# Kernel tuning notes

Hardware: AMD Instinct MI355X
Metric: run time of the kernel (lower is better)

The kernel has to match this reference:

```python
import jax, jax.numpy as jnp
import numpy as np

NX, NH, NY, T = 128, 512, 1, 16384


def setup_inputs() -> dict:
    key = jax.random.key(0)
    ks = jax.random.split(key, 10)
    s = 0.01
    return {
        "x_t": jax.random.normal(ks[0], (T, 1), dtype=jnp.float32),
        "Wf": jax.random.normal(ks[1], (NH, NX), dtype=jnp.float32) * s,
        "Uf": jax.random.normal(ks[2], (NH, NH), dtype=jnp.float32) * s,
        "bf": jnp.zeros((NH,), dtype=jnp.float32),
        "Wi": jax.random.normal(ks[3], (NH, NX), dtype=jnp.float32) * s,
        "Ui": jax.random.normal(ks[4], (NH, NH), dtype=jnp.float32) * s,
        "bi": jnp.zeros((NH,), dtype=jnp.float32),
        "Wo": jax.random.normal(ks[5], (NH, NX), dtype=jnp.float32) * s,
        "Uo": jax.random.normal(ks[6], (NH, NH), dtype=jnp.float32) * s,
        "bo": jnp.zeros((NH,), dtype=jnp.float32),
        "Wc": jax.random.normal(ks[7], (NH, NX), dtype=jnp.float32) * s,
        "Uc": jax.random.normal(ks[8], (NH, NH), dtype=jnp.float32) * s,
        "bc": jnp.zeros((NH,), dtype=jnp.float32),
        "Ahy": jax.random.normal(ks[9], (NY, NH), dtype=jnp.float32) * s,
        "by": jnp.zeros((NY,), dtype=jnp.float32),
    }


def reference(x_t, Wf, Uf, bf, Wi, Ui, bi, Wo, Uo, bo, Wc, Uc, bc, Ahy, by):
    # x_t: (T, 1) univariate series; sliding windows of length Nx feed each step.
    Tlen = x_t.shape[0]
    Nx = Wf.shape[1]
    Nh = Wf.shape[0]
    steps = Tlen - Nx  # number of recurrent steps

    x = x_t[:, 0]  # (T,)
    idx = jnp.arange(steps)[:, None] + jnp.arange(Nx)[None, :]
    Xw = x[idx]  # (steps, Nx) sliding windows

    # Precompute input projections for all steps (batched GEMMs).
    xf = Xw @ Wf.T + bf  # (steps, Nh)
    xi = Xw @ Wi.T + bi
    xo = Xw @ Wo.T + bo
    xc = Xw @ Wc.T + bc

    def step(carry, inp):
        h, c = carry
        xf_t, xi_t, xo_t, xc_t = inp
        f = jax.nn.sigmoid(xf_t + Uf @ h)
        i = jax.nn.sigmoid(xi_t + Ui @ h)
        o = jax.nn.sigmoid(xo_t + Uo @ h)
        g = jnp.tanh(xc_t + Uc @ h)
        c = f * c + i * g
        h = o * jnp.tanh(c)
        mu = Ahy @ h + by  # (Ny,)
        return (h, c), mu

    init = (jnp.zeros((Nh,), x_t.dtype), jnp.zeros((Nh,), x_t.dtype))
    _, mu = jax.lax.scan(step, init, (xf, xi, xo, xc))
    return mu  # (steps, Ny) == (T-Nx, 1), matching torch's stack(...).unsqueeze(1)
```

## Files before the change

kernel.cpp:

```cpp
#include <hip/hip_runtime.h>

#define NHID 512
#define NXW  128
#define TLEN 16384
#define STEPS (TLEN - NXW)
#define G    32
#define B    512
#define RPW  16
#define RSLOTS 8

#define FOR4(M)  M(0) M(1) M(2) M(3)
#define FOR16(M) M(0) M(1) M(2) M(3) M(4) M(5) M(6) M(7) \
                 M(8) M(9) M(10) M(11) M(12) M(13) M(14) M(15)

__device__ __forceinline__ float sigmoid_f(float v) { return 1.f / (1.f + __expf(-v)); }
__device__ __forceinline__ float tanh_f(float v)    { return 1.f - 2.f / (1.f + __expf(2.f * v)); }

#define AWR(dst, src) asm volatile("v_accvgpr_write_b32 %0, %1" : "=a"(dst) : "v"(src));
#define ARD(dst, src) asm volatile("v_accvgpr_read_b32 %0, %1" : "=v"(dst) : "a"(src));

__launch_bounds__(B, 2)
__global__ void lstm_persistent(
    const float* x,
    const float* Wf, const float* Uf, const float* bf,
    const float* Wi, const float* Ui, const float* bi,
    const float* Wo, const float* Uo, const float* bo,
    const float* Wc, const float* Uc, const float* bc,
    unsigned long long* ring,
    float* h_hist)
{
    __shared__ float x_win[256];
    __shared__ __align__(16) float h_buf[8][64];
    __shared__ float partials[2][B];

    const int tid = threadIdx.x;
    const int g   = blockIdx.x;
    const int w   = tid >> 6;
    const int l   = tid & 63;
    const int q   = l >> 4;
    const int row = g * RPW + (l & 15);

    const float* Utab[4] = {Uf, Ui, Uo, Uc};
    const float* Wtab[4] = {Wf, Wi, Wo, Wc};
    const float* Btab[4] = {bf, bi, bo, bc};

    const float4* Up = (const float4*)(Utab[q] + (size_t)row * NHID + w * 64);
    #define LOADU(i) float a##i##x, a##i##y, a##i##z, a##i##w;              \
        { float4 tmp = Up[i];                                               \
          AWR(a##i##x, tmp.x) AWR(a##i##y, tmp.y)                           \
          AWR(a##i##z, tmp.z) AWR(a##i##w, tmp.w) }
    FOR16(LOADU)

    const float4* Wp = (const float4*)(Wtab[q] + row * NXW + w * 16);
    #define DECLW(i) float4 wv##i = Wp[i];
    FOR4(DECLW)
    #define PIN(r) asm volatile("" : "+v"(r.x), "+v"(r.y), "+v"(r.z), "+v"(r.w));
    #define PINW(i) PIN(wv##i)
    FOR4(PINW)

    float bias = 0.f, c_prev = 0.f;
    if (w == 0) bias = Btab[q][row];

    const bool hist_writer = (w == (g >> 2)) && ((l >> 4) == (g & 3));

    h_buf[w][l] = 0.f;

    for (int t = 0; t < STEPS; ++t) {
        if ((t & 127) == 0) {
            __syncthreads();
            if (tid < 256) {
                int gi = t + tid;
                x_win[tid] = (gi < TLEN) ? x[gi] : 0.f;
            }
            __syncthreads();
        }

        float xacc = 0.f;
        {
            const int xb = (t & 127) + w * 16;
            #define XF(i) xacc += wv##i.x * x_win[xb + 4*i]     \
                                + wv##i.y * x_win[xb + 4*i + 1] \
                                + wv##i.z * x_win[xb + 4*i + 2] \
                                + wv##i.w * x_win[xb + 4*i + 3];
            FOR4(XF)
        }

        float hval = 0.f;
        if (t > 0) {
            const unsigned long long* src =
                ring + ((size_t)((t - 1) & (RSLOTS - 1)) << 9) + (w * 64 + l);
            const unsigned want = (unsigned)(t - 1);
            unsigned long long vv; int guard = 0;
            do {
                vv = __hip_atomic_load(src, __ATOMIC_RELAXED, __HIP_MEMORY_SCOPE_AGENT);
            } while ((unsigned)(vv >> 32) != want && ++guard < (1 << 20));
            hval = __uint_as_float((unsigned)vv);
            h_buf[w][l] = hval;
        }

        float acc = xacc;
        const float4* hb4 = (const float4*)h_buf[w];
        #define UF(i) { float4 hv = hb4[i]; float t0, t1, t2, t3;           \
                        ARD(t0, a##i##x) ARD(t1, a##i##y)                   \
                        ARD(t2, a##i##z) ARD(t3, a##i##w)                   \
                        acc += t0 * hv.x + t1 * hv.y                        \
                             + t2 * hv.z + t3 * hv.w; }
        FOR16(UF)
        partials[t & 1][(w << 6) | l] = acc;

        if (t > 0 && hist_writer)
            h_hist[(size_t)(t - 1) * NHID + w * 64 + l] = hval;

        __syncthreads();

        if (w == 0) {
            const float* p = partials[t & 1];
            float pre = acc + bias;
            #pragma unroll
            for (int s2 = 1; s2 < 8; ++s2) pre += p[s2 * 64 + l];
            float a = (l < 48) ? sigmoid_f(pre) : tanh_f(pre);
            float ai = __shfl(a, l + 16, 64);
            float ao = __shfl(a, l + 32, 64);
            float ag = __shfl(a, l + 48, 64);
            if (l < 16) {
                float c = a * c_prev + ai * ag;
                c_prev = c;
                float h = ao * tanh_f(c);
                unsigned long long pv =
                    ((unsigned long long)(unsigned)t << 32)
                    | (unsigned long long)__float_as_uint(h);
                __hip_atomic_store(
                    ring + ((size_t)(t & (RSLOTS - 1)) << 9) + row, pv,
                    __ATOMIC_RELAXED, __HIP_MEMORY_SCOPE_AGENT);
                if (t == STEPS - 1)
                    h_hist[(size_t)t * NHID + row] = h;
            }
        }
    }
}

__global__ void mu_kernel(const float* __restrict__ h_hist,
                          const float* __restrict__ Ahy,
                          const float* __restrict__ by,
                          float* __restrict__ outp, int steps)
{
    int wave = threadIdx.x >> 6;
    int lane = threadIdx.x & 63;
    int t = blockIdx.x * 4 + wave;
    if (t >= steps) return;
    const float* h = h_hist + (size_t)t * NHID;
    float p = 0.f;
    #pragma unroll
    for (int e = 0; e < 8; e++)
        p += Ahy[e * 64 + lane] * h[e * 64 + lane];
    #pragma unroll
    for (int off = 32; off; off >>= 1) p += __shfl_down(p, off, 64);
    if (lane == 0) outp[t] = p + by[0];
}

extern "C" void kernel_launch(void* const* d_in, const int* in_sizes, int n_in,
                              void* d_out, int out_size, void* d_ws, size_t ws_size,
                              hipStream_t stream)
{
    const float* x  = (const float*)d_in[0];
    const float* Wf = (const float*)d_in[1];
    const float* Uf = (const float*)d_in[2];
    const float* bf = (const float*)d_in[3];
    const float* Wi = (const float*)d_in[4];
    const float* Ui = (const float*)d_in[5];
    const float* bi = (const float*)d_in[6];
    const float* Wo = (const float*)d_in[7];
    const float* Uo = (const float*)d_in[8];
    const float* bo = (const float*)d_in[9];
    const float* Wc = (const float*)d_in[10];
    const float* Uc = (const float*)d_in[11];
    const float* bc = (const float*)d_in[12];
    const float* Ahy = (const float*)d_in[13];
    const float* by  = (const float*)d_in[14];

    unsigned long long* ring = (unsigned long long*)d_ws;
    float* h_hist = (float*)((char*)d_ws + RSLOTS * NHID * 8);

    lstm_persistent<<<G, B, 0, stream>>>(x, Wf, Uf, bf, Wi, Ui, bi,
                                         Wo, Uo, bo, Wc, Uc, bc, ring, h_hist);
    int muBlocks = (STEPS + 3) / 4;
    mu_kernel<<<muBlocks, 256, 0, stream>>>(h_hist, Ahy, by, (float*)d_out, STEPS);
}
```

Baseline: 27.01 ms.

## Halve persistent LSTM workgroups to 16 with 1024 threads each

Restructures the persistent recurrent kernel to use 16 workgroups of 1024 threads, each owning 32 hidden rows instead of 16. Two waves share each 64-column slice of h. Only one of each pair polls the global ring and fills shared memory, followed by an extra barrier. The goal is to cut the number of blocks polling the cross-block ring each step, and so the global synchronisation traffic. The cost is an extra __syncthreads per step and more work per block on the serial critical path.

```diff
diff --git a/kernel.cpp b/kernel.cpp
--- a/kernel.cpp
+++ b/kernel.cpp
@@ -4,9 +4,9 @@
 #define NXW  128
 #define TLEN 16384
 #define STEPS (TLEN - NXW)
-#define G    32
-#define B    512
-#define RPW  16
+#define G    16
+#define B    1024
+#define RPW  32
 #define RSLOTS 8
 
 #define FOR4(M)  M(0) M(1) M(2) M(3)
@@ -19,7 +19,7 @@
 #define AWR(dst, src) asm volatile("v_accvgpr_write_b32 %0, %1" : "=a"(dst) : "v"(src));
 #define ARD(dst, src) asm volatile("v_accvgpr_read_b32 %0, %1" : "=v"(dst) : "a"(src));
 
-__launch_bounds__(B, 2)
+__launch_bounds__(B)
 __global__ void lstm_persistent(
     const float* x,
     const float* Wf, const float* Uf, const float* bf,
@@ -31,39 +31,43 @@
 {
     __shared__ float x_win[256];
     __shared__ __align__(16) float h_buf[8][64];
-    __shared__ float partials[2][B];
+    __shared__ float partials[2][8][128];
 
-    const int tid = threadIdx.x;
-    const int g   = blockIdx.x;
-    const int w   = tid >> 6;
-    const int l   = tid & 63;
-    const int q   = l >> 4;
-    const int row = g * RPW + (l & 15);
+    const int tid  = threadIdx.x;
+    const int g    = blockIdx.x;
+    const int w    = tid >> 6;
+    const int l    = tid & 63;
+    const int s    = w >> 1;
+    const int half = w & 1;
+    const int q    = l >> 4;
+    const int r    = l & 15;
+    const int row  = g * RPW + half * 16 + r;
+    const int outw = q * 32 + half * 16 + r;
 
     const float* Utab[4] = {Uf, Ui, Uo, Uc};
     const float* Wtab[4] = {Wf, Wi, Wo, Wc};
     const float* Btab[4] = {bf, bi, bo, bc};
 
-    const float4* Up = (const float4*)(Utab[q] + (size_t)row * NHID + w * 64);
+    const float4* Up = (const float4*)(Utab[q] + (size_t)row * NHID + s * 64);
     #define LOADU(i) float a##i##x, a##i##y, a##i##z, a##i##w;              \
         { float4 tmp = Up[i];                                               \
           AWR(a##i##x, tmp.x) AWR(a##i##y, tmp.y)                           \
           AWR(a##i##z, tmp.z) AWR(a##i##w, tmp.w) }
     FOR16(LOADU)
 
-    const float4* Wp = (const float4*)(Wtab[q] + row * NXW + w * 16);
+    const float4* Wp = (const float4*)(Wtab[q] + row * NXW + s * 16);
     #define DECLW(i) float4 wv##i = Wp[i];
     FOR4(DECLW)
-    #define PIN(r) asm volatile("" : "+v"(r.x), "+v"(r.y), "+v"(r.z), "+v"(r.w));
+    #define PIN(v) asm volatile("" : "+v"(v.x), "+v"(v.y), "+v"(v.z), "+v"(v.w));
     #define PINW(i) PIN(wv##i)
     FOR4(PINW)
 
     float bias = 0.f, c_prev = 0.f;
-    if (w == 0) bias = Btab[q][row];
+    if (w < 2) bias = Btab[q][row];
 
-    const bool hist_writer = (w == (g >> 2)) && ((l >> 4) == (g & 3));
+    const bool hist_writer = (half == 0) && (s == (g >> 1)) && ((l >> 5) == (g & 1));
 
-    h_buf[w][l] = 0.f;
+    if (half == 0) h_buf[s][l] = 0.f;
 
     for (int t = 0; t < STEPS; ++t) {
         if ((t & 127) == 0) {
@@ -77,7 +81,7 @@
 
         float xacc = 0.f;
         {
-            const int xb = (t & 127) + w * 16;
+            const int xb = (t & 127) + s * 16;
             #define XF(i) xacc += wv##i.x * x_win[xb + 4*i]     \
                                 + wv##i.y * x_win[xb + 4*i + 1] \
                                 + wv##i.z * x_win[xb + 4*i + 2] \
@@ -86,54 +90,56 @@
         }
 
         float hval = 0.f;
-        if (t > 0) {
+        if (t > 0 && half == 0) {
             const unsigned long long* src =
-                ring + ((size_t)((t - 1) & (RSLOTS - 1)) << 9) + (w * 64 + l);
+                ring + ((size_t)((t - 1) & (RSLOTS - 1)) << 9) + (s * 64 + l);
             const unsigned want = (unsigned)(t - 1);
             unsigned long long vv; int guard = 0;
             do {
                 vv = __hip_atomic_load(src, __ATOMIC_RELAXED, __HIP_MEMORY_SCOPE_AGENT);
             } while ((unsigned)(vv >> 32) != want && ++guard < (1 << 20));
             hval = __uint_as_float((unsigned)vv);
-            h_buf[w][l] = hval;
+            h_buf[s][l] = hval;
         }
+        __syncthreads();
 
         float acc = xacc;
-        const float4* hb4 = (const float4*)h_buf[w];
+        const float4* hb4 = (const float4*)h_buf[s];
         #define UF(i) { float4 hv = hb4[i]; float t0, t1, t2, t3;           \
                         ARD(t0, a##i##x) ARD(t1, a##i##y)                   \
                         ARD(t2, a##i##z) ARD(t3, a##i##w)                   \
                         acc += t0 * hv.x + t1 * hv.y                        \
                              + t2 * hv.z + t3 * hv.w; }
         FOR16(UF)
-        partials[t & 1][(w << 6) | l] = acc;
+        partials[t & 1][s][outw] = acc;
 
         if (t > 0 && hist_writer)
-            h_hist[(size_t)(t - 1) * NHID + w * 64 + l] = hval;
+            h_hist[(size_t)(t - 1) * NHID + s * 64 + l] = hval;
 
         __syncthreads();
 
-        if (w == 0) {
-            const float* p = partials[t & 1];
+        if (w < 2) {
             float pre = acc + bias;
             #pragma unroll
-            for (int s2 = 1; s2 < 8; ++s2) pre += p[s2 * 64 + l];
+            for (int s2 = 1; s2 < 8; ++s2) pre += partials[t & 1][s2][outw];
             float a = (l < 48) ? sigmoid_f(pre) : tanh_f(pre);
-            float ai = __shfl(a, l + 16, 64);
-            float ao = __shfl(a, l + 32, 64);
-            float ag = __shfl(a, l + 48, 64);
+            float fA = __shfl(a, r,      64);
+            float iA = __shfl(a, 16 + r, 64);
+            float oA = __shfl(a, 32 + r, 64);
+            float gA = __shfl(a, 48 + r, 64);
             if (l < 16) {
-                float c = a * c_prev + ai * ag;
+                float c = fA * c_prev + iA * gA;
                 c_prev = c;
-                float h = ao * tanh_f(c);
+                float h = oA * tanh_f(c);
+                const int trow = g * RPW + w * 16 + l;
                 unsigned long long pv =
                     ((unsigned long long)(unsigned)t << 32)
                     | (unsigned long long)__float_as_uint(h);
                 __hip_atomic_store(
-                    ring + ((size_t)(t & (RSLOTS - 1)) << 9) + row, pv,
+                    ring + ((size_t)(t & (RSLOTS - 1)) << 9) + trow, pv,
                     __ATOMIC_RELAXED, __HIP_MEMORY_SCOPE_AGENT);
                 if (t == STEPS - 1)
-                    h_hist[(size_t)t * NHID + row] = h;
+                    h_hist[(size_t)t * NHID + trow] = h;
             }
         }
     }
```

Measured after the change: 33.85 ms. 25.3% more time.
